# Optimization experiments

Measured on AMD Instinct MI355X. Metric: run time of the kernel, lower is better.

## Reference

```python
import jax, jax.numpy as jnp
import numpy as np

B, N, H, D, DEPTH = 16, 1024, 2, 128, 3
A = H * D  # atten_dim = 256
FFN = 1024
EPS = 1e-5


def layer_norm(x, g, b):
    mu = jnp.mean(x, axis=-1, keepdims=True)
    var = jnp.mean(jnp.square(x - mu), axis=-1, keepdims=True)
    return (x - mu) * jax.lax.rsqrt(var + EPS) * g + b


def setup_inputs() -> dict:
    key = jax.random.key(0)
    ks = jax.random.split(key, 16)
    s = lambda fan_in: 1.0 / np.sqrt(fan_in)
    inp = {
        "X": jax.random.normal(ks[0], (B, N, A), jnp.float32),
        # per-layer attention projections, stacked over depth
        "Wq": jax.random.normal(ks[1], (DEPTH, A, A), jnp.float32) * s(A),
        "bq": jnp.zeros((DEPTH, A), jnp.float32),
        "Wk": jax.random.normal(ks[2], (DEPTH, A, A), jnp.float32) * s(A),
        "bk": jnp.zeros((DEPTH, A), jnp.float32),
        "Wv": jax.random.normal(ks[3], (DEPTH, A, A), jnp.float32) * s(A),
        "bv": jnp.zeros((DEPTH, A), jnp.float32),
        # per-layer FFN (roll_out): Linear(A,1024)+ReLU, Linear(1024,A)+ReLU
        "W1": jax.random.normal(ks[4], (DEPTH, A, FFN), jnp.float32) * s(A),
        "b1": jnp.zeros((DEPTH, FFN), jnp.float32),
        "W2": jax.random.normal(ks[5], (DEPTH, FFN, A), jnp.float32) * s(FFN),
        "b2": jnp.zeros((DEPTH, A), jnp.float32),
        # single shared LayerNorm (the torch module reuses one instance)
        "ln_g": jnp.ones((A,), jnp.float32),
        "ln_b": jnp.zeros((A,), jnp.float32),
        # Conv1d(A, A, kernel_size=1) == per-position linear over channels
        "Wc": jax.random.normal(ks[6], (A, A), jnp.float32) * s(A),
        "bc": jnp.zeros((A,), jnp.float32),
        # final Linear(A, A) on pooled features
        "We": jax.random.normal(ks[7], (A, A), jnp.float32) * s(A),
        "be": jnp.zeros((A,), jnp.float32),
    }
    return inp


def reference(X, Wq, bq, Wk, bk, Wv, bv, W1, b1, W2, b2, ln_g, ln_b, Wc, bc, We, be):
    inv_sqrt_d = 1.0 / np.sqrt(D)
    step = X  # [B, N, A]
    for i in range(DEPTH):
        q = (step @ Wq[i] + bq[i]).reshape(B, N, H, D).transpose(0, 2, 1, 3)
        k = (step @ Wk[i] + bk[i]).reshape(B, N, H, D).transpose(0, 2, 1, 3)
        v = (step @ Wv[i] + bv[i]).reshape(B, N, H, D).transpose(0, 2, 1, 3)
        scores = jnp.einsum('bhqd,bhkd->bhqk', q, k) * inv_sqrt_d
        probs = jax.nn.softmax(scores, axis=-1)
        attn = jnp.einsum('bhqk,bhkd->bhqd', probs, v)
        attn = attn.transpose(0, 2, 1, 3).reshape(B, N, A)
        roll = jax.nn.relu(jax.nn.relu(attn @ W1[i] + b1[i]) @ W2[i] + b2[i])
        step = layer_norm(roll + step, ln_g, ln_b)
    # Conv1d(kernel=1) + ReLU over channels, per position
    entity_encodings = jax.nn.relu(step @ Wc + bc)  # [B, N, A]
    pooled = jnp.mean(entity_encodings, axis=1)      # [B, A]
    encoded_entities = jax.nn.relu(pooled @ We + be)  # [B, A]
    return encoded_entities
```

## Files before the change

kernel.cpp:

```cpp
#include <hip/hip_runtime.h>
#include <hip/hip_bf16.h>
#include <cstddef>

#define B_   16
#define N_   1024
#define H_   2
#define D_   128
#define A_   256
#define FFN_ 1024
#define M_   (B_ * N_)
#define EPS_ 1e-5f
#define SPLIT 4
#define KT   32
#define TPC  (N_ / SPLIT / KT)
#define QKV_E ((size_t)B_ * H_ * N_ * D_)

typedef short  short8  __attribute__((ext_vector_type(8)));
typedef float  f32x16  __attribute__((ext_vector_type(16)));
typedef unsigned int uint;
typedef unsigned short ushort;

#define MFMA32(a, b, c) __builtin_amdgcn_mfma_f32_32x32x16_bf16(a, b, c, 0, 0, 0)

__device__ __forceinline__ uint f2b1(float x) {
    uint u = __float_as_uint(x);
    return (u + 0x7fffu + ((u >> 16) & 1u)) >> 16;
}
__device__ __forceinline__ uint f2b2(float lo, float hi) {
    return f2b1(lo) | (f2b1(hi) << 16);
}
__device__ __forceinline__ float b2f(ushort u) {
    return __uint_as_float(((uint)u) << 16);
}

__global__ __launch_bounds__(256) void f32_to_bf16_kernel(
    const float* __restrict__ in, ushort* __restrict__ out)
{
    const size_t i = ((size_t)blockIdx.x * 256 + threadIdx.x) * 8;
    float4 a = *(const float4*)(in + i);
    float4 b = *(const float4*)(in + i + 4);
    uint4 w = { f2b2(a.x, a.y), f2b2(a.z, a.w), f2b2(b.x, b.y), f2b2(b.z, b.w) };
    *(uint4*)(out + i) = w;
}

__global__ __launch_bounds__(256) void prep_kernel(
    const float* __restrict__ Wq, const float* __restrict__ Wk,
    const float* __restrict__ Wv, const float* __restrict__ W1,
    const float* __restrict__ W2, const float* __restrict__ Wc,
    ushort* __restrict__ wqkv_t, ushort* __restrict__ w1_t,
    ushort* __restrict__ w2_t, ushort* __restrict__ wc_t)
{
    const int z = blockIdx.z;
    const float* W; ushort* out; int K, N, n0, k0;
    if (z < 9) {
        const int layer = z / 3, sec = z % 3;
        W = (sec == 0 ? Wq : sec == 1 ? Wk : Wv) + (size_t)layer * A_ * A_;
        out = wqkv_t + (size_t)layer * 3 * A_ * A_ + (size_t)sec * A_ * A_;
        K = A_; N = A_;
        n0 = blockIdx.x * 32; k0 = blockIdx.y * 32;
    } else if (z < 12) {
        const int layer = z - 9;
        W = W1 + (size_t)layer * A_ * FFN_; out = w1_t + (size_t)layer * A_ * FFN_;
        K = A_; N = FFN_;
        n0 = blockIdx.x * 32; k0 = blockIdx.y * 32;
    } else if (z < 15) {
        const int layer = z - 12;
        W = W2 + (size_t)layer * FFN_ * A_; out = w2_t + (size_t)layer * FFN_ * A_;
        K = FFN_; N = A_;
        k0 = blockIdx.x * 32; n0 = blockIdx.y * 32;
    } else {
        W = Wc; out = wc_t; K = A_; N = A_;
        n0 = blockIdx.x * 32; k0 = blockIdx.y * 32;
    }
    if (n0 >= N || k0 >= K) return;

    __shared__ float tile[32][33];
    const int tc = threadIdx.x & 31, tr = threadIdx.x >> 5;
#pragma unroll
    for (int it = 0; it < 4; ++it) {
        int r = it * 8 + tr;
        tile[r][tc] = W[(size_t)(k0 + r) * N + n0 + tc];
    }
    __syncthreads();
#pragma unroll
    for (int it = 0; it < 4; ++it) {
        int r = it * 8 + tr;
        out[(size_t)(n0 + r) * K + k0 + tc] = (ushort)f2b1(tile[tc][r]);
    }
}

template <int MR>
__global__ __launch_bounds__(256) void gemm_mfma(
    const ushort* __restrict__ Asrc, const ushort* __restrict__ Wt,
    const float* __restrict__ bias, const float* __restrict__ biasK,
    const float* __restrict__ biasV, void* __restrict__ outp,
    int Kloop, int lda, int ldc, int mode)
{
    constexpr int BM = MR * 64;
    __shared__ ushort sA[BM * 72];
    __shared__ ushort sB[128 * 72];

    const int tid = threadIdx.x;
    const int wid = tid >> 6, lane = tid & 63;
    const int c = lane & 31, g = lane >> 5;
    const int wr = wid >> 1, wc = wid & 1;
    const int m0 = blockIdx.x * BM;
    const int n0 = blockIdx.y * 128;

    size_t zout = 0;
    if (mode == 7) {
        const int h = blockIdx.z;
        Asrc += (size_t)h * Kloop;
        Wt   += (size_t)h * Kloop;
        zout  = (size_t)h * M_ * A_;
    }

    f32x16 acc[MR][2] = {};

    for (int k0 = 0; k0 < Kloop; k0 += 64) {
        __syncthreads();
#pragma unroll
        for (int it = 0; it < BM / 32; ++it) {
            int idx = it * 256 + tid, r = idx >> 3, cc = (idx & 7) * 8;
            *(uint4*)&sA[r * 72 + cc] =
                *(const uint4*)(Asrc + (size_t)(m0 + r) * lda + k0 + cc);
        }
#pragma unroll
        for (int it = 0; it < 4; ++it) {
            int idx = it * 256 + tid, r = idx >> 3, cc = (idx & 7) * 8;
            *(uint4*)&sB[r * 72 + cc] =
                *(const uint4*)(Wt + (size_t)(n0 + r) * lda + k0 + cc);
        }
        __syncthreads();
#pragma unroll
        for (int ks = 0; ks < 4; ++ks) {
            const int ko = ks * 16 + 8 * g;
            short8 b0 = *(const short8*)&sB[(wc * 64 + c) * 72 + ko];
            short8 b1 = *(const short8*)&sB[(wc * 64 + 32 + c) * 72 + ko];
#pragma unroll
            for (int mr = 0; mr < MR; ++mr) {
                short8 a = *(const short8*)&sA[((wr * MR + mr) * 32 + c) * 72 + ko];
                acc[mr][0] = MFMA32(a, b0, acc[mr][0]);
                acc[mr][1] = MFMA32(a, b1, acc[mr][1]);
            }
        }
    }

    const int sec = n0 >> 8;
    const float* bp = bias;
    int nw = n0;
    if (mode == 5) {
        bp = (sec == 0 ? bias : sec == 1 ? biasK : biasV);
        nw = n0 & 255;
    }
    const float bz[2] = { bp[nw + wc * 64 + c], bp[nw + wc * 64 + 32 + c] };

    float colsum[2] = { 0.f, 0.f };

#pragma unroll
    for (int mr = 0; mr < MR; ++mr) {
#pragma unroll
        for (int ct = 0; ct < 2; ++ct) {
            const int colbase = n0 + wc * 64 + ct * 32 + c;
            const float addb = (mode == 7) ? 0.f : bz[ct];
#pragma unroll
            for (int rg = 0; rg < 4; ++rg) {
                const int row = m0 + (wr * MR + mr) * 32 + 8 * rg + 4 * g;
                float v0 = acc[mr][ct][4 * rg + 0] + addb;
                float v1 = acc[mr][ct][4 * rg + 1] + addb;
                float v2 = acc[mr][ct][4 * rg + 2] + addb;
                float v3 = acc[mr][ct][4 * rg + 3] + addb;
                if (mode == 1 || mode == 2 || mode == 6) {
                    v0 = fmaxf(v0, 0.f); v1 = fmaxf(v1, 0.f);
                    v2 = fmaxf(v2, 0.f); v3 = fmaxf(v3, 0.f);
                }
                if (mode == 1) {
                    float* o = (float*)outp;
                    o[(size_t)(row + 0) * ldc + colbase] = v0;
                    o[(size_t)(row + 1) * ldc + colbase] = v1;
                    o[(size_t)(row + 2) * ldc + colbase] = v2;
                    o[(size_t)(row + 3) * ldc + colbase] = v3;
                } else if (mode == 2 || mode == 7) {
                    ushort* o = (ushort*)outp + zout;
                    o[(size_t)(row + 0) * ldc + colbase] = (ushort)f2b1(v0);
                    o[(size_t)(row + 1) * ldc + colbase] = (ushort)f2b1(v1);
                    o[(size_t)(row + 2) * ldc + colbase] = (ushort)f2b1(v2);
                    o[(size_t)(row + 3) * ldc + colbase] = (ushort)f2b1(v3);
                } else if (mode == 6) {
                    colsum[ct] += v0 + v1 + v2 + v3;
                } else {
                    const int cw = colbase & 255;
                    const int hh = cw >> 7, dd = cw & (D_ - 1);
                    if (sec < 2) {
                        ushort* o = (ushort*)outp + (size_t)sec * QKV_E;
#pragma unroll
                        for (int r2 = 0; r2 < 4; ++r2) {
                            int rw = row + r2;
                            int bb = rw >> 10, np = rw & (N_ - 1);
                            float vv = (r2 == 0 ? v0 : r2 == 1 ? v1 : r2 == 2 ? v2 : v3);
                            size_t off = (((size_t)(bb * H_ + hh) * 32 + (np >> 5)) * 16
                                          + (dd >> 3)) * 256
                                         + (np & 31) * 8 + (dd & 7);
                            o[off] = (ushort)f2b1(vv);
                        }
                    } else {
                        ushort* o = (ushort*)outp + 2 * QKV_E;
                        const int bb = row >> 10, np = row & (N_ - 1);
                        size_t off = ((((size_t)(bb * H_ + hh) * 32 + (np >> 5)) * 4
                                       + (dd >> 5)) * 4 + ((np & 31) >> 3)) * 256
                                     + (dd & 31) * 8 + (np & 7);
                        uint2 w = { f2b2(v0, v1), f2b2(v2, v3) };
                        *(uint2*)(o + off) = w;
                    }
                }
            }
        }
    }

    if (mode == 6) {
        float* part = (float*)outp;
        const int b = m0 >> 10;
#pragma unroll
        for (int ct = 0; ct < 2; ++ct) {
            float cs = colsum[ct] + __shfl_xor(colsum[ct], 32, 64);
            if (g == 0)
                atomicAdd(&part[(size_t)b * A_ + n0 + wc * 64 + ct * 32 + c], cs);
        }
    }
}

#define OPITCH 132

__global__ __launch_bounds__(128, 2) void attn_kernel(
    const ushort* __restrict__ qg, const ushort* __restrict__ kg,
    const ushort* __restrict__ vtg, ushort* __restrict__ po,
    float* __restrict__ pm, float* __restrict__ pl)
{
    __shared__ ushort sO[64 * OPITCH];

    const int tid = threadIdx.x;
    const int w = tid >> 6, lane = tid & 63;
    const int c = lane & 31, g = lane >> 5;

    const int flat = blockIdx.x;
    const int xcd  = flat & 7;
    const int ii   = flat >> 3;
    const int pair = xcd * 16 + (ii & 15);
    const int qt   = ii >> 4;
    const int bh   = pair & 31;
    const int z    = pair >> 5;

    const int q0 = qt * 64 + w * 32;
    const float scale2 = 0.08838834764831845f * 1.44269504f;
    const float THR = 11.5f;
    const int lo8 = c * 8;

    short8 qf[8];
    const ushort* qt_ = qg + ((size_t)bh * 32 + (q0 >> 5)) * 4096;
#pragma unroll
    for (int ks = 0; ks < 8; ++ks)
        qf[ks] = *(const short8*)(qt_ + (2 * ks + g) * 256 + lo8);

    f32x16 oacc[4] = {};
    float m = -1e30f, l = 0.f;

    const size_t chunk0 = ((size_t)bh * 32 + z * 8) * 4096;
    const ushort* kb0 = kg + chunk0 + g * 256 + lo8;
    short8 kf0 = *(const short8*)(kb0 + 0 * 512);
    short8 kf1 = *(const short8*)(kb0 + 1 * 512);
    short8 kf2 = *(const short8*)(kb0 + 2 * 512);
    short8 kf3 = *(const short8*)(kb0 + 3 * 512);
    short8 kf4 = *(const short8*)(kb0 + 4 * 512);
    short8 kf5 = *(const short8*)(kb0 + 5 * 512);
    short8 kf6 = *(const short8*)(kb0 + 6 * 512);
    short8 kf7 = *(const short8*)(kb0 + 7 * 512);

    for (int t = 0; t < TPC; ++t) {
        const size_t tb = chunk0 + (size_t)t * 4096;

        const ushort* vb = vtg + tb + g * 256 + lo8;
        short8 vfA0 = *(const short8*)(vb + 0 * 1024);
        short8 vfA1 = *(const short8*)(vb + 1 * 1024);
        short8 vfA2 = *(const short8*)(vb + 2 * 1024);
        short8 vfA3 = *(const short8*)(vb + 3 * 1024);
        short8 vfB0 = *(const short8*)(vb + 0 * 1024 + 512);
        short8 vfB1 = *(const short8*)(vb + 1 * 1024 + 512);
        short8 vfB2 = *(const short8*)(vb + 2 * 1024 + 512);
        short8 vfB3 = *(const short8*)(vb + 3 * 1024 + 512);
        __builtin_amdgcn_sched_barrier(0);

        f32x16 sacc = {};
        __builtin_amdgcn_s_setprio(1);
        sacc = MFMA32(kf0, qf[0], sacc);
        sacc = MFMA32(kf1, qf[1], sacc);
        sacc = MFMA32(kf2, qf[2], sacc);
        sacc = MFMA32(kf3, qf[3], sacc);
        sacc = MFMA32(kf4, qf[4], sacc);
        sacc = MFMA32(kf5, qf[5], sacc);
        sacc = MFMA32(kf6, qf[6], sacc);
        sacc = MFMA32(kf7, qf[7], sacc);
        __builtin_amdgcn_s_setprio(0);

        if (t + 1 < TPC) {
            const ushort* kb2 = kg + tb + 4096 + g * 256 + lo8;
            kf0 = *(const short8*)(kb2 + 0 * 512);
            kf1 = *(const short8*)(kb2 + 1 * 512);
            kf2 = *(const short8*)(kb2 + 2 * 512);
            kf3 = *(const short8*)(kb2 + 3 * 512);
            kf4 = *(const short8*)(kb2 + 4 * 512);
            kf5 = *(const short8*)(kb2 + 5 * 512);
            kf6 = *(const short8*)(kb2 + 6 * 512);
            kf7 = *(const short8*)(kb2 + 7 * 512);
        }
        __builtin_amdgcn_sched_barrier(0);

        float p[16];
        float tmax = -1e30f;
#pragma unroll
        for (int r = 0; r < 16; ++r) {
            float s = sacc[r] * scale2;
            p[r] = s;
            tmax = fmaxf(tmax, s);
        }
        tmax = fmaxf(tmax, __shfl_xor(tmax, 32, 64));
        if (!__all(tmax - m <= THR)) {
            const float mnew = fmaxf(m, tmax);
            const float corr = exp2f(m - mnew);
#pragma unroll
            for (int dt = 0; dt < 4; ++dt)
#pragma unroll
                for (int r = 0; r < 16; ++r) oacc[dt][r] *= corr;
            l *= corr;
            m = mnew;
        }
        float tsum = 0.f;
#pragma unroll
        for (int r = 0; r < 16; ++r) {
            p[r] = exp2f(p[r] - m);
            tsum += p[r];
        }
        tsum += __shfl_xor(tsum, 32, 64);
        l += tsum;

        uint pk[8];
#pragma unroll
        for (int pp = 0; pp < 8; ++pp)
            pk[pp] = f2b2(p[2 * pp], p[2 * pp + 1]);

        uint v0 = g ? pk[0] : pk[2];
        uint v1 = g ? pk[1] : pk[3];
        uint v2 = g ? pk[4] : pk[6];
        uint v3 = g ? pk[5] : pk[7];
        uint r0 = (uint)__shfl_xor((int)v0, 32, 64);
        uint r1 = (uint)__shfl_xor((int)v1, 32, 64);
        uint r2 = (uint)__shfl_xor((int)v2, 32, 64);
        uint r3 = (uint)__shfl_xor((int)v3, 32, 64);

        __builtin_amdgcn_s_setprio(1);
#pragma unroll
        for (int kb = 0; kb < 2; ++kb) {
            union { uint u[4]; short8 s; } pf;
            if (kb == 0) {
                pf.u[0] = g ? r0 : pk[0];
                pf.u[1] = g ? r1 : pk[1];
                pf.u[2] = g ? pk[2] : r0;
                pf.u[3] = g ? pk[3] : r1;
            } else {
                pf.u[0] = g ? r2 : pk[4];
                pf.u[1] = g ? r3 : pk[5];
                pf.u[2] = g ? pk[6] : r2;
                pf.u[3] = g ? pk[7] : r3;
            }
            oacc[0] = MFMA32(kb ? vfB0 : vfA0, pf.s, oacc[0]);
            oacc[1] = MFMA32(kb ? vfB1 : vfA1, pf.s, oacc[1]);
            oacc[2] = MFMA32(kb ? vfB2 : vfA2, pf.s, oacc[2]);
            oacc[3] = MFMA32(kb ? vfB3 : vfA3, pf.s, oacc[3]);
        }
        __builtin_amdgcn_s_setprio(0);
    }

    if (lane < 32) {
        pm[(size_t)(z * 32 + bh) * N_ + q0 + c] = m;
        pl[(size_t)(z * 32 + bh) * N_ + q0 + c] = l;
    }
    {
        const int qrl = w * 32 + c;
#pragma unroll
        for (int dt = 0; dt < 4; ++dt)
#pragma unroll
            for (int rg = 0; rg < 4; ++rg) {
                int d = dt * 32 + 8 * rg + 4 * g;
                uint2 pv = { f2b2(oacc[dt][4 * rg + 0], oacc[dt][4 * rg + 1]),
                             f2b2(oacc[dt][4 * rg + 2], oacc[dt][4 * rg + 3]) };
                *(uint2*)&sO[qrl * OPITCH + d] = pv;
            }
    }
    __syncthreads();
    {
        const size_t pbase = ((size_t)(z * 32 + bh) * N_ + qt * 64) * D_;
#pragma unroll
        for (int it = 0; it < 16; ++it) {
            int idx = it * 128 + tid;
            int r = idx >> 5, dgr = (idx & 31) * 4;
            uint2 v = *(const uint2*)&sO[r * OPITCH + dgr];
            *(uint2*)(po + pbase + (size_t)r * D_ + dgr) = v;
        }
    }
}

__global__ __launch_bounds__(256) void combine_kernel(
    const ushort* __restrict__ po, const float* __restrict__ pm,
    const float* __restrict__ pl, ushort* __restrict__ out)
{
    const int idx = blockIdx.x * 256 + threadIdx.x;
    const int row = idx >> 4, d0 = (idx & 15) * 8;
    const int R = B_ * H_ * N_;

    float ms[SPLIT];
    float M = -1e30f;
#pragma unroll
    for (int s = 0; s < SPLIT; ++s) {
        ms[s] = pm[(size_t)s * R + row];
        M = fmaxf(M, ms[s]);
    }
    float L = 0.f;
    float acc[8] = {};
#pragma unroll
    for (int s = 0; s < SPLIT; ++s) {
        float wgt = exp2f(ms[s] - M);
        L += pl[(size_t)s * R + row] * wgt;
        uint4 pv = *(const uint4*)(po + ((size_t)s * R + row) * D_ + d0);
        const ushort* pu = (const ushort*)&pv;
#pragma unroll
        for (int j = 0; j < 8; ++j) acc[j] += b2f(pu[j]) * wgt;
    }
    const float inv = 1.f / L;
    uint4 w;
    w.x = f2b2(acc[0] * inv, acc[1] * inv);
    w.y = f2b2(acc[2] * inv, acc[3] * inv);
    w.z = f2b2(acc[4] * inv, acc[5] * inv);
    w.w = f2b2(acc[6] * inv, acc[7] * inv);
    const int bh = row >> 10, n = row & (N_ - 1);
    const int bb = bh >> 1, hh = bh & 1;
    *(uint4*)(out + ((size_t)(bb * N_ + n)) * A_ + hh * D_ + d0) = w;
}

__global__ __launch_bounds__(256) void add_ln_kernel(
    const ushort* __restrict__ roll0, const ushort* __restrict__ roll1,
    const float* __restrict__ b2, ushort* __restrict__ stepb,
    const float* __restrict__ g, const float* __restrict__ bta)
{
    const int row = blockIdx.x * 4 + (threadIdx.x >> 6);
    const int lane = threadIdx.x & 63, c4 = lane * 4;
    const size_t base = (size_t)row * A_ + c4;

    uint2 ra = *(const uint2*)(roll0 + base);
    uint2 rb = *(const uint2*)(roll1 + base);
    uint2 pb = *(const uint2*)(stepb + base);
    float4 bz = *(const float4*)(b2 + c4);

    float r0 = fmaxf(b2f((ushort)(ra.x & 0xffff)) + b2f((ushort)(rb.x & 0xffff)) + bz.x, 0.f);
    float r1 = fmaxf(b2f((ushort)(ra.x >> 16))    + b2f((ushort)(rb.x >> 16))    + bz.y, 0.f);
    float r2 = fmaxf(b2f((ushort)(ra.y & 0xffff)) + b2f((ushort)(rb.y & 0xffff)) + bz.z, 0.f);
    float r3 = fmaxf(b2f((ushort)(ra.y >> 16))    + b2f((ushort)(rb.y >> 16))    + bz.w, 0.f);

    float v0 = r0 + b2f((ushort)(pb.x & 0xffff));
    float v1 = r1 + b2f((ushort)(pb.x >> 16));
    float v2 = r2 + b2f((ushort)(pb.y & 0xffff));
    float v3 = r3 + b2f((ushort)(pb.y >> 16));

    float s  = v0 + v1 + v2 + v3;
    float s2 = v0 * v0 + v1 * v1 + v2 * v2 + v3 * v3;
#pragma unroll
    for (int o = 32; o > 0; o >>= 1) {
        s  += __shfl_xor(s, o, 64);
        s2 += __shfl_xor(s2, o, 64);
    }
    const float mu = s * (1.f / A_);
    const float rs = rsqrtf(s2 * (1.f / A_) - mu * mu + EPS_);

    float4 gv = *(const float4*)(g + c4);
    float4 bv = *(const float4*)(bta + c4);
    float y0 = (v0 - mu) * rs * gv.x + bv.x;
    float y1 = (v1 - mu) * rs * gv.y + bv.y;
    float y2 = (v2 - mu) * rs * gv.z + bv.z;
    float y3 = (v3 - mu) * rs * gv.w + bv.w;

    uint2 yb = { f2b2(y0, y1), f2b2(y2, y3) };
    *(uint2*)(stepb + base) = yb;
}

__global__ __launch_bounds__(256) void final_kernel(
    const float* __restrict__ part, const float* __restrict__ We,
    const float* __restrict__ be, float* __restrict__ out)
{
    __shared__ float sp[A_];
    const int b = blockIdx.x, tid = threadIdx.x;
    sp[tid] = part[(size_t)b * A_ + tid] * (1.0f / N_);
    __syncthreads();
    float acc = be[tid];
    for (int kk = 0; kk < A_; ++kk) acc += sp[kk] * We[(size_t)kk * A_ + tid];
    out[b * A_ + tid] = fmaxf(acc, 0.f);
}

extern "C" void kernel_launch(void* const* d_in, const int* in_sizes, int n_in,
                              void* d_out, int out_size, void* d_ws, size_t ws_size,
                              hipStream_t stream)
{
    const float* X    = (const float*)d_in[0];
    const float* Wq   = (const float*)d_in[1];
    const float* bq   = (const float*)d_in[2];
    const float* Wk   = (const float*)d_in[3];
    const float* bk   = (const float*)d_in[4];
    const float* Wv   = (const float*)d_in[5];
    const float* bv   = (const float*)d_in[6];
    const float* W1   = (const float*)d_in[7];
    const float* b1   = (const float*)d_in[8];
    const float* W2   = (const float*)d_in[9];
    const float* b2   = (const float*)d_in[10];
    const float* ln_g = (const float*)d_in[11];
    const float* ln_b = (const float*)d_in[12];
    const float* Wc   = (const float*)d_in[13];
    const float* bc   = (const float*)d_in[14];
    const float* We   = (const float*)d_in[15];
    const float* be   = (const float*)d_in[16];

    char* base = (char*)d_ws;
    ushort* qb     = (ushort*)base;  base += QKV_E * 2;
                             base += QKV_E * 2;
                             base += QKV_E * 2;
    ushort* hbuf   = (ushort*)base;  base += (size_t)M_ * FFN_ * 2;
    ushort* rollp  = (ushort*)base;  base += (size_t)2 * M_ * A_ * 2;
    ushort* stepb  = (ushort*)base;  base += (size_t)M_ * A_ * 2;
    ushort* wqkv_t = (ushort*)base;  base += (size_t)3 * 3 * A_ * A_ * 2;
    ushort* w1_t   = (ushort*)base;  base += (size_t)3 * A_ * FFN_ * 2;
    ushort* w2_t   = (ushort*)base;  base += (size_t)3 * FFN_ * A_ * 2;
    ushort* wc_t   = (ushort*)base;  base += (size_t)A_ * A_ * 2;
    float*  part   = (float*)base;   base += (size_t)B_ * A_ * 4;
    float*  pm     = (float*)base;   base += (size_t)SPLIT * B_ * H_ * N_ * 4;
    float*  pl     = (float*)base;   base += (size_t)SPLIT * B_ * H_ * N_ * 4;
    ushort* kbuf   = qb + QKV_E;
    ushort* vtbuf  = qb + 2 * QKV_E;
    ushort* po     = hbuf;
    ushort* attnb  = qb;

    prep_kernel<<<dim3(32, 8, 16), 256, 0, stream>>>(
        Wq, Wk, Wv, W1, W2, Wc, wqkv_t, w1_t, w2_t, wc_t);
    f32_to_bf16_kernel<<<(M_ * A_) / (256 * 8), 256, 0, stream>>>(X, stepb);

    for (int i = 0; i < 3; ++i) {
        gemm_mfma<2><<<dim3(M_/128, 6), 256, 0, stream>>>(
            stepb, wqkv_t + (size_t)i * 3 * A_ * A_,
            bq + i * A_, bk + i * A_, bv + i * A_, qb, A_, A_, 0, 5);

        attn_kernel<<<16 * SPLIT * B_ * H_, 128, 0, stream>>>(
            qb, kbuf, vtbuf, po, pm, pl);
        combine_kernel<<<(B_*H_*N_*D_)/(256*8), 256, 0, stream>>>(po, pm, pl, attnb);

        gemm_mfma<2><<<dim3(M_/128, FFN_/128), 256, 0, stream>>>(
            attnb, w1_t + (size_t)i * A_ * FFN_, b1 + i * FFN_, nullptr, nullptr,
            hbuf, A_, A_, FFN_, 2);
        gemm_mfma<1><<<dim3(M_/64, A_/128, 2), 256, 0, stream>>>(
            hbuf, w2_t + (size_t)i * FFN_ * A_, b2 + i * A_, nullptr, nullptr,
            rollp, FFN_/2, FFN_, A_, 7);

        add_ln_kernel<<<M_/4, 256, 0, stream>>>(
            rollp, rollp + (size_t)M_ * A_, b2 + i * A_, stepb, ln_g, ln_b);
    }

    hipMemsetAsync(part, 0, (size_t)B_ * A_ * 4, stream);
    gemm_mfma<1><<<dim3(M_/64, A_/128), 256, 0, stream>>>(
        stepb, wc_t, bc, nullptr, nullptr, part, A_, A_, 0, 6);
    final_kernel<<<B_, 256, 0, stream>>>(part, We, be, (float*)d_out);
}
```

Baseline: 363.7 us.

## Software-pipeline QK^T MFMAs one tile ahead of softmax in attention loop

```diff
diff --git a/kernel.cpp b/kernel.cpp
--- a/kernel.cpp
+++ b/kernel.cpp
@@ -265,119 +265,140 @@
     float m = -1e30f, l = 0.f;
 
     const size_t chunk0 = ((size_t)bh * 32 + z * 8) * 4096;
-    const ushort* kb0 = kg + chunk0 + g * 256 + lo8;
-    short8 kf0 = *(const short8*)(kb0 + 0 * 512);
-    short8 kf1 = *(const short8*)(kb0 + 1 * 512);
-    short8 kf2 = *(const short8*)(kb0 + 2 * 512);
-    short8 kf3 = *(const short8*)(kb0 + 3 * 512);
-    short8 kf4 = *(const short8*)(kb0 + 4 * 512);
-    short8 kf5 = *(const short8*)(kb0 + 5 * 512);
-    short8 kf6 = *(const short8*)(kb0 + 6 * 512);
-    short8 kf7 = *(const short8*)(kb0 + 7 * 512);
-
-    for (int t = 0; t < TPC; ++t) {
-        const size_t tb = chunk0 + (size_t)t * 4096;
-
-        const ushort* vb = vtg + tb + g * 256 + lo8;
-        short8 vfA0 = *(const short8*)(vb + 0 * 1024);
-        short8 vfA1 = *(const short8*)(vb + 1 * 1024);
-        short8 vfA2 = *(const short8*)(vb + 2 * 1024);
-        short8 vfA3 = *(const short8*)(vb + 3 * 1024);
-        short8 vfB0 = *(const short8*)(vb + 0 * 1024 + 512);
-        short8 vfB1 = *(const short8*)(vb + 1 * 1024 + 512);
-        short8 vfB2 = *(const short8*)(vb + 2 * 1024 + 512);
-        short8 vfB3 = *(const short8*)(vb + 3 * 1024 + 512);
-        __builtin_amdgcn_sched_barrier(0);
-
-        f32x16 sacc = {};
-        __builtin_amdgcn_s_setprio(1);
-        sacc = MFMA32(kf0, qf[0], sacc);
-        sacc = MFMA32(kf1, qf[1], sacc);
-        sacc = MFMA32(kf2, qf[2], sacc);
-        sacc = MFMA32(kf3, qf[3], sacc);
-        sacc = MFMA32(kf4, qf[4], sacc);
-        sacc = MFMA32(kf5, qf[5], sacc);
-        sacc = MFMA32(kf6, qf[6], sacc);
-        sacc = MFMA32(kf7, qf[7], sacc);
-        __builtin_amdgcn_s_setprio(0);
-
-        if (t + 1 < TPC) {
-            const ushort* kb2 = kg + tb + 4096 + g * 256 + lo8;
-            kf0 = *(const short8*)(kb2 + 0 * 512);
-            kf1 = *(const short8*)(kb2 + 1 * 512);
-            kf2 = *(const short8*)(kb2 + 2 * 512);
-            kf3 = *(const short8*)(kb2 + 3 * 512);
-            kf4 = *(const short8*)(kb2 + 4 * 512);
-            kf5 = *(const short8*)(kb2 + 5 * 512);
-            kf6 = *(const short8*)(kb2 + 6 * 512);
-            kf7 = *(const short8*)(kb2 + 7 * 512);
-        }
-        __builtin_amdgcn_sched_barrier(0);
-
-        float p[16];
-        float tmax = -1e30f;
-#pragma unroll
-        for (int r = 0; r < 16; ++r) {
-            float s = sacc[r] * scale2;
-            p[r] = s;
-            tmax = fmaxf(tmax, s);
-        }
-        tmax = fmaxf(tmax, __shfl_xor(tmax, 32, 64));
-        if (!__all(tmax - m <= THR)) {
-            const float mnew = fmaxf(m, tmax);
-            const float corr = exp2f(m - mnew);
-#pragma unroll
-            for (int dt = 0; dt < 4; ++dt)
-#pragma unroll
-                for (int r = 0; r < 16; ++r) oacc[dt][r] *= corr;
-            l *= corr;
-            m = mnew;
-        }
-        float tsum = 0.f;
-#pragma unroll
-        for (int r = 0; r < 16; ++r) {
-            p[r] = exp2f(p[r] - m);
-            tsum += p[r];
-        }
-        tsum += __shfl_xor(tsum, 32, 64);
-        l += tsum;
-
-        uint pk[8];
-#pragma unroll
-        for (int pp = 0; pp < 8; ++pp)
-            pk[pp] = f2b2(p[2 * pp], p[2 * pp + 1]);
-
-        uint v0 = g ? pk[0] : pk[2];
-        uint v1 = g ? pk[1] : pk[3];
-        uint v2 = g ? pk[4] : pk[6];
-        uint v3 = g ? pk[5] : pk[7];
-        uint r0 = (uint)__shfl_xor((int)v0, 32, 64);
-        uint r1 = (uint)__shfl_xor((int)v1, 32, 64);
-        uint r2 = (uint)__shfl_xor((int)v2, 32, 64);
-        uint r3 = (uint)__shfl_xor((int)v3, 32, 64);
-
-        __builtin_amdgcn_s_setprio(1);
-#pragma unroll
-        for (int kb = 0; kb < 2; ++kb) {
-            union { uint u[4]; short8 s; } pf;
-            if (kb == 0) {
-                pf.u[0] = g ? r0 : pk[0];
-                pf.u[1] = g ? r1 : pk[1];
-                pf.u[2] = g ? pk[2] : r0;
-                pf.u[3] = g ? pk[3] : r1;
-            } else {
-                pf.u[0] = g ? r2 : pk[4];
-                pf.u[1] = g ? r3 : pk[5];
-                pf.u[2] = g ? pk[6] : r2;
-                pf.u[3] = g ? pk[7] : r3;
-            }
-            oacc[0] = MFMA32(kb ? vfB0 : vfA0, pf.s, oacc[0]);
-            oacc[1] = MFMA32(kb ? vfB1 : vfA1, pf.s, oacc[1]);
-            oacc[2] = MFMA32(kb ? vfB2 : vfA2, pf.s, oacc[2]);
-            oacc[3] = MFMA32(kb ? vfB3 : vfA3, pf.s, oacc[3]);
-        }
-        __builtin_amdgcn_s_setprio(0);
-    }
+
+    short8 kf0, kf1, kf2, kf3, kf4, kf5, kf6, kf7;
+    {
+        const ushort* kb0 = kg + chunk0 + g * 256 + lo8;
+        kf0 = *(const short8*)(kb0 + 0 * 512);
+        kf1 = *(const short8*)(kb0 + 1 * 512);
+        kf2 = *(const short8*)(kb0 + 2 * 512);
+        kf3 = *(const short8*)(kb0 + 3 * 512);
+        kf4 = *(const short8*)(kb0 + 4 * 512);
+        kf5 = *(const short8*)(kb0 + 5 * 512);
+        kf6 = *(const short8*)(kb0 + 6 * 512);
+        kf7 = *(const short8*)(kb0 + 7 * 512);
+    }
+    f32x16 saccA = {}, saccB = {};
+    saccA = MFMA32(kf0, qf[0], saccA);
+    saccA = MFMA32(kf1, qf[1], saccA);
+    saccA = MFMA32(kf2, qf[2], saccA);
+    saccA = MFMA32(kf3, qf[3], saccA);
+    saccA = MFMA32(kf4, qf[4], saccA);
+    saccA = MFMA32(kf5, qf[5], saccA);
+    saccA = MFMA32(kf6, qf[6], saccA);
+    saccA = MFMA32(kf7, qf[7], saccA);
+
+#define ATTN_BODY(T, CUR, NXT)                                                 \
+    {                                                                          \
+        const size_t tb = chunk0 + (size_t)(T) * 4096;                         \
+                                     \
+        const ushort* vb = vtg + tb + g * 256 + lo8;                           \
+        short8 vfA0 = *(const short8*)(vb + 0 * 1024);                         \
+        short8 vfA1 = *(const short8*)(vb + 1 * 1024);                         \
+        short8 vfA2 = *(const short8*)(vb + 2 * 1024);                         \
+        short8 vfA3 = *(const short8*)(vb + 3 * 1024);                         \
+        short8 vfB0 = *(const short8*)(vb + 0 * 1024 + 512);                   \
+        short8 vfB1 = *(const short8*)(vb + 1 * 1024 + 512);                   \
+        short8 vfB2 = *(const short8*)(vb + 2 * 1024 + 512);                   \
+        short8 vfB3 = *(const short8*)(vb + 3 * 1024 + 512);                   \
+                          \
+        if ((T) + 1 < TPC) {                                                   \
+            const ushort* kb2 = kg + tb + 4096 + g * 256 + lo8;                \
+            kf0 = *(const short8*)(kb2 + 0 * 512);                             \
+            kf1 = *(const short8*)(kb2 + 1 * 512);                             \
+            kf2 = *(const short8*)(kb2 + 2 * 512);                             \
+            kf3 = *(const short8*)(kb2 + 3 * 512);                             \
+            kf4 = *(const short8*)(kb2 + 4 * 512);                             \
+            kf5 = *(const short8*)(kb2 + 5 * 512);                             \
+            kf6 = *(const short8*)(kb2 + 6 * 512);                             \
+            kf7 = *(const short8*)(kb2 + 7 * 512);                             \
+        }                                                                      \
+        __builtin_amdgcn_sched_barrier(0);                                     \
+                         \
+        float p[16];                                                           \
+        float tmax = -1e30f;                                                   \
+        _Pragma("unroll")                                                      \
+        for (int r = 0; r < 16; ++r) {                                         \
+            float s = CUR[r] * scale2;                                         \
+            p[r] = s;                                                          \
+            tmax = fmaxf(tmax, s);                                             \
+        }                                                                      \
+        tmax = fmaxf(tmax, __shfl_xor(tmax, 32, 64));                          \
+        if (!__all(tmax - m <= THR)) {                                         \
+            const float mnew = fmaxf(m, tmax);                                 \
+            const float corr = exp2f(m - mnew);                                \
+            _Pragma("unroll")                                                  \
+            for (int dt = 0; dt < 4; ++dt)                                     \
+                _Pragma("unroll")                                              \
+                for (int r = 0; r < 16; ++r) oacc[dt][r] *= corr;              \
+            l *= corr;                                                         \
+            m = mnew;                                                          \
+        }                                                                      \
+        float tsum = 0.f;                                                      \
+        _Pragma("unroll")                                                      \
+        for (int r = 0; r < 16; ++r) {                                         \
+            p[r] = exp2f(p[r] - m);                                            \
+            tsum += p[r];                                                      \
+        }                                                                      \
+        tsum += __shfl_xor(tsum, 32, 64);                                      \
+        l += tsum;                                                             \
+           \
+        if ((T) + 1 < TPC) {                                                   \
+            NXT = (f32x16){};                                                  \
+            NXT = MFMA32(kf0, qf[0], NXT);                                     \
+            NXT = MFMA32(kf1, qf[1], NXT);                                     \
+            NXT = MFMA32(kf2, qf[2], NXT);                                     \
+            NXT = MFMA32(kf3, qf[3], NXT);                                     \
+            NXT = MFMA32(kf4, qf[4], NXT);                                     \
+            NXT = MFMA32(kf5, qf[5], NXT);                                     \
+            NXT = MFMA32(kf6, qf[6], NXT);                                     \
+            NXT = MFMA32(kf7, qf[7], NXT);                                     \
+        }                                                                      \
+                \
+        uint pk[8];                                                            \
+        _Pragma("unroll")                                                      \
+        for (int pp = 0; pp < 8; ++pp)                                         \
+            pk[pp] = f2b2(p[2 * pp], p[2 * pp + 1]);                           \
+        uint x0 = g ? pk[0] : pk[2];                                           \
+        uint x1 = g ? pk[1] : pk[3];                                           \
+        uint x2 = g ? pk[4] : pk[6];                                           \
+        uint x3 = g ? pk[5] : pk[7];                                           \
+        uint r0 = (uint)__shfl_xor((int)x0, 32, 64);                           \
+        uint r1 = (uint)__shfl_xor((int)x1, 32, 64);                           \
+        uint r2 = (uint)__shfl_xor((int)x2, 32, 64);                           \
+        uint r3 = (uint)__shfl_xor((int)x3, 32, 64);                           \
+                                                                    \
+        __builtin_amdgcn_s_setprio(1);                                         \
+        {                                                                      \
+            union { uint u[4]; short8 s; } pf;                                 \
+            pf.u[0] = g ? r0 : pk[0];                                          \
+            pf.u[1] = g ? r1 : pk[1];                                          \
+            pf.u[2] = g ? pk[2] : r0;                                          \
+            pf.u[3] = g ? pk[3] : r1;                                          \
+            oacc[0] = MFMA32(vfA0, pf.s, oacc[0]);                             \
+            oacc[1] = MFMA32(vfA1, pf.s, oacc[1]);                             \
+            oacc[2] = MFMA32(vfA2, pf.s, oacc[2]);                             \
+            oacc[3] = MFMA32(vfA3, pf.s, oacc[3]);                             \
+        }                                                                      \
+        {                                                                      \
+            union { uint u[4]; short8 s; } pf;                                 \
+            pf.u[0] = g ? r2 : pk[4];                                          \
+            pf.u[1] = g ? r3 : pk[5];                                          \
+            pf.u[2] = g ? pk[6] : r2;                                          \
+            pf.u[3] = g ? pk[7] : r3;                                          \
+            oacc[0] = MFMA32(vfB0, pf.s, oacc[0]);                             \
+            oacc[1] = MFMA32(vfB1, pf.s, oacc[1]);                             \
+            oacc[2] = MFMA32(vfB2, pf.s, oacc[2]);                             \
+            oacc[3] = MFMA32(vfB3, pf.s, oacc[3]);                             \
+        }                                                                      \
+        __builtin_amdgcn_s_setprio(0);                                         \
+    }
+
+    for (int tt = 0; tt < TPC; tt += 2) {
+        ATTN_BODY(tt,     saccA, saccB)
+        ATTN_BODY(tt + 1, saccB, saccA)
+    }
+#undef ATTN_BODY
 
     if (lane < 32) {
         pm[(size_t)(z * 32 + bh) * N_ + q0 + c] = m;
```

Result: no change. 366.6 us (+0.8%).
